# Kernel tuning notes

Measured on AMD Instinct MI355X. Metric: run time of the kernel, lower is better.

## Reference

```python
import jax, jax.numpy as jnp
import numpy as np

BS, P, D = 64, 300, 1024
NUM_CLASSES = 150


def setup_inputs() -> dict:
    key = jax.random.key(0)
    ks = jax.random.split(key, 12)
    s = 0.02
    return {
        "x": jax.random.normal(ks[0], (BS * P, D), jnp.float32),
        "subject": jax.random.normal(ks[1], (BS, D), jnp.float32),
        "obj": jax.random.normal(ks[2], (BS, D), jnp.float32),
        "relation": jax.random.normal(ks[3], (BS, D), jnp.float32),
        "W_theta": jax.random.normal(ks[4], (D, D), jnp.float32) * s,
        "b_theta": jax.random.normal(ks[5], (D,), jnp.float32) * s,
        "W_pair": jax.random.normal(ks[6], (3 * D, 1), jnp.float32) * s,
        "b_pair": jax.random.normal(ks[7], (1,), jnp.float32) * s,
        "W_cls": jax.random.normal(ks[8], (2 * D, 1), jnp.float32) * s,
        "b_cls": jax.random.normal(ks[9], (1,), jnp.float32) * s,
        "W_bbox": jax.random.normal(ks[10], (D, (NUM_CLASSES + 1) * 4), jnp.float32) * s,
        "b_bbox": jax.random.normal(ks[11], ((NUM_CLASSES + 1) * 4,), jnp.float32) * s,
    }


def reference(x, subject, obj, relation, W_theta, b_theta, W_pair, b_pair,
              W_cls, b_cls, W_bbox, b_bbox):
    bs = relation.shape[0]
    rel = relation @ W_theta + b_theta  # (bs, D)
    xb = x.reshape(bs, P, D)

    # cls_score_pair(concat([x1, x2, rel])) decomposed into 3 sliced matmuls.
    # x1[b,i,j] = x[b,j] (cols), x2[b,i,j] = x[b,i] (rows).
    Wa, Wb, Wc = W_pair[:D, 0], W_pair[D:2 * D, 0], W_pair[2 * D:, 0]
    col_term = xb @ Wa          # (bs, P) -> broadcast over rows i
    row_term = xb @ Wb          # (bs, P) -> broadcast over cols j
    rel_term = rel @ Wc + b_pair[0]  # (bs,)
    pair_score = jax.nn.sigmoid(row_term[:, :, None] + col_term[None if False else slice(None), None, :]
                                + rel_term[:, None, None])  # (bs, P, P)

    # cls_score on [x, subject] and [x, object]
    W1, W2 = W_cls[:D, 0], W_cls[D:, 0]
    xw = xb @ W1                                  # (bs, P)
    s_score = jax.nn.sigmoid(xw + (subject @ W2 + b_cls[0])[:, None])  # (bs, P)
    o_score = jax.nn.sigmoid(xw + (obj @ W2 + b_cls[0])[:, None])      # (bs, P)

    pair_score = pair_score * o_score[:, None, :] * s_score[:, :, None]

    x_subj = jnp.stack([1.0 - s_score, s_score], axis=-1).reshape(-1, 2)
    x_obj = jnp.stack([1.0 - o_score, o_score], axis=-1).reshape(-1, 2)

    bbox_deltas = x @ W_bbox + b_bbox  # (bs*P, (C+1)*4)
    return (x_subj, x_obj, pair_score, bbox_deltas)
```

## Files before the change

kernel.cpp:

```cpp
#include <hip/hip_runtime.h>

#define PP    300
#define DD    1024
#define NOUT  604
#define NROWS 19200
#define OFF_PAIR  76800
#define OFF_BBOX  5836800

typedef unsigned short u16;
typedef __attribute__((ext_vector_type(8))) short bf16x8;
typedef __attribute__((ext_vector_type(4))) float f32x4;

#define GLOBAL_AS __attribute__((address_space(1)))
#define LDS_AS    __attribute__((address_space(3)))

__device__ inline u16 f2bf(float f) {
    unsigned u = __float_as_uint(f);
    return (u16)((u + 0x7fffu + ((u >> 16) & 1u)) >> 16);
}
__device__ inline float dot4(float4 a, float4 b) {
    return fmaf(a.x, b.x, fmaf(a.y, b.y, fmaf(a.z, b.z, a.w * b.w)));
}
__device__ inline float sigmoidf(float z) { return 1.f / (1.f + __expf(-z)); }

__global__ void k_vtheta(const float* __restrict__ Wt, const float* __restrict__ Wpair,
                         float* __restrict__ v) {
    int wave = threadIdx.x >> 6, lane = threadIdx.x & 63;
    int k = blockIdx.x * 4 + wave;
    const float4* row = (const float4*)(Wt + (size_t)k * DD);
    const float4* wc  = (const float4*)(Wpair + 2 * DD);
    float s = 0.f;
#pragma unroll
    for (int i = 0; i < 4; ++i) s += dot4(row[i * 64 + lane], wc[i * 64 + lane]);
#pragma unroll
    for (int off = 32; off; off >>= 1) s += __shfl_down(s, off, 64);
    if (lane == 0) v[k] = s;
}

__global__ void k_scalars(const float* __restrict__ relation, const float* __restrict__ subject,
                          const float* __restrict__ obj, const float* __restrict__ btheta,
                          const float* __restrict__ Wpair, const float* __restrict__ bpair,
                          const float* __restrict__ Wcls, const float* __restrict__ bcls,
                          const float* __restrict__ v,
                          float* __restrict__ relt, float* __restrict__ subc,
                          float* __restrict__ objc) {
    __shared__ float red[4];
    int wave = threadIdx.x >> 6, lane = threadIdx.x & 63;
    int b = blockIdx.x;
    const float4* aa;
    const float4* bb;
    if (wave == 0)      { aa = (const float4*)(relation + (size_t)b * DD); bb = (const float4*)v; }
    else if (wave == 1) { aa = (const float4*)(subject + (size_t)b * DD);  bb = (const float4*)(Wcls + DD); }
    else if (wave == 2) { aa = (const float4*)(obj + (size_t)b * DD);      bb = (const float4*)(Wcls + DD); }
    else                { aa = (const float4*)btheta;                      bb = (const float4*)(Wpair + 2 * DD); }
    float s = 0.f;
#pragma unroll
    for (int i = 0; i < 4; ++i) s += dot4(aa[i * 64 + lane], bb[i * 64 + lane]);
#pragma unroll
    for (int off = 32; off; off >>= 1) s += __shfl_down(s, off, 64);
    if (lane == 0) red[wave] = s;
    __syncthreads();
    if (threadIdx.x == 0) {
        relt[b] = red[0] + red[3] + bpair[0];
        subc[b] = red[1] + bcls[0];
        objc[b] = red[2] + bcls[0];
    }
}

template<int WB>
__global__ __launch_bounds__(256) void k_rows_t(
        const float* __restrict__ x, const float* __restrict__ Wpair,
        const float* __restrict__ Wcls,
        const float* __restrict__ relt, const float* __restrict__ subc,
        const float* __restrict__ objc,
        float* __restrict__ colv, float* __restrict__ rowp,
        float* __restrict__ sarr, float* __restrict__ oarr,
        float* __restrict__ out, u16* __restrict__ xb,
        const float* __restrict__ Wbbox, u16* __restrict__ Bt) {
    __shared__ float tile[32][33];
    if (blockIdx.x >= 4800) {
        int blk = blockIdx.x - 4800;
        int tid = threadIdx.x;
        int k0 = (blk & 31) * 32;
        int n0 = (blk >> 5) * 32;
        int tx = tid & 31;
        int ty = tid >> 5;
#pragma unroll
        for (int i = 0; i < 4; ++i) {
            int k = k0 + ty + i * 8;
            int n = n0 + tx;
            tile[ty + i * 8][tx] = (n < NOUT) ? Wbbox[(size_t)k * NOUT + n] : 0.f;
        }
        __syncthreads();
#pragma unroll
        for (int i = 0; i < 4; ++i) {
            int n = n0 + ty + i * 8;
            int k = k0 + tx;
            Bt[(size_t)n * DD + k] = f2bf(tile[tx][ty + i * 8]);
        }
        return;
    }
    int wave = threadIdx.x >> 6, lane = threadIdx.x & 63;
    int r = blockIdx.x * 4 + wave;
    const float4* xr = (const float4*)(x + (size_t)r * DD);
    const float4* wa = (const float4*)(Wpair);
    const float4* wb = (const float4*)(Wpair + DD);
    const float4* w1 = (const float4*)(Wcls);
    float ca = 0.f, cb = 0.f, cw = 0.f;
#pragma unroll
    for (int i = 0; i < 4; ++i) {
        int idx = i * 64 + lane;
        float4 xv = xr[idx];
        ca += dot4(xv, wa[idx]);
        cb += dot4(xv, wb[idx]);
        cw += dot4(xv, w1[idx]);
        if (WB) {
            unsigned lo = __builtin_amdgcn_perm(__float_as_uint(xv.y), __float_as_uint(xv.x), 0x07060302u);
            unsigned hi = __builtin_amdgcn_perm(__float_as_uint(xv.w), __float_as_uint(xv.z), 0x07060302u);
            *(uint2*)(xb + (size_t)r * DD + idx * 4) = make_uint2(lo, hi);
        }
    }
#pragma unroll
    for (int off = 32; off; off >>= 1) {
        ca += __shfl_down(ca, off, 64);
        cb += __shfl_down(cb, off, 64);
        cw += __shfl_down(cw, off, 64);
    }
    if (lane == 0) {
        int b = r / 300;
        float s = sigmoidf(cw + subc[b]);
        float o = sigmoidf(cw + objc[b]);
        colv[r] = ca;
        rowp[r] = cb + relt[b];
        sarr[r] = s;
        oarr[r] = o;
        ((float2*)out)[r]         = make_float2(1.f - s, s);
        ((float2*)out)[NROWS + r] = make_float2(1.f - o, o);
    }
}

#define BKK 64
#define NSTEP 16

#define WAITCNT_VM(N) asm volatile("s_waitcnt vmcnt(" #N ")" ::: "memory")

#define STAGE_TILE(buf, k0)                                                                  \
    _Pragma("unroll")                                                                        \
    for (int q = 0; q < 4; ++q) {                                                            \
        int rowblk = q * 32 + wave * 8;                                                      \
        const u16* ga = a_base + (size_t)(rowblk + s_row) * DD + (k0) + s_c16 * 8;           \
        __builtin_amdgcn_global_load_lds((const GLOBAL_AS unsigned int*)ga,                  \
                                         (LDS_AS unsigned int*)(As[buf] + rowblk * BKK),     \
                                         16, 0, 0);                                          \
        const u16* gb = b_base + (size_t)(rowblk + s_row) * DD + (k0) + s_c16 * 8;           \
        __builtin_amdgcn_global_load_lds((const GLOBAL_AS unsigned int*)gb,                  \
                                         (LDS_AS unsigned int*)(Bs[buf] + rowblk * BKK),     \
                                         16, 0, 0);                                          \
    }

#define COMPUTE_TILE(buf)                                                                    \
    _Pragma("unroll")                                                                        \
    for (int kk = 0; kk < BKK; kk += 32) {                                                   \
        bf16x8 af[4], bfv[4];                                                                \
        int cx = (((kk >> 3) + quad) ^ (l16 & 7)) * 8;                                       \
        _Pragma("unroll")                                                                    \
        for (int f = 0; f < 4; ++f) {                                                        \
            int m = wr * 64 + f * 16 + l16;                                                  \
            af[f] = *(const bf16x8*)(As[buf] + m * BKK + cx);                                \
            int n = wc * 64 + f * 16 + l16;                                                  \
            bfv[f] = *(const bf16x8*)(Bs[buf] + n * BKK + cx);                               \
        }                                                                                    \
        _Pragma("unroll")                                                                    \
        for (int fi = 0; fi < 4; ++fi)                                                       \
            _Pragma("unroll")                                                                \
            for (int fj = 0; fj < 4; ++fj)                                                   \
                acc[fi][fj] = __builtin_amdgcn_mfma_f32_16x16x32_bf16(                       \
                    af[fi], bfv[fj], acc[fi][fj], 0, 0, 0);                                  \
    }

__global__ __launch_bounds__(256) void k_fused(
        const u16* __restrict__ xb, const u16* __restrict__ bt,
        const float* __restrict__ bias, float* __restrict__ outb,
        const float* __restrict__ rowp, const float* __restrict__ colv,
        const float* __restrict__ sarr, const float* __restrict__ oarr,
        float* __restrict__ pout) {
    __shared__ u16 As[2][128 * BKK] __attribute__((aligned(16)));
    __shared__ u16 Bs[2][128 * BKK] __attribute__((aligned(16)));

    int gbid = blockIdx.x;
    if (gbid < 760) {
        int xcd = gbid & 7;
        int rest = gbid >> 3;
        int n_t = rest % 5;
        int m_t = (rest / 5) * 8 + xcd;
        if (m_t >= 150) return;

        int tid = threadIdx.x;
        int wave = tid >> 6;
        int lane = tid & 63;
        int wr = wave >> 1, wc = wave & 1;
        int quad = lane >> 4;
        int l16 = lane & 15;

        f32x4 acc[4][4] = {};

        const u16* a_base = xb + (size_t)m_t * 128 * DD;
        const u16* b_base = bt + (size_t)n_t * 128 * DD;
        int s_row = lane >> 3;
        int s_c16 = (lane & 7) ^ s_row;

        STAGE_TILE(0, 0)

#pragma unroll 1
        for (int t = 0; t < NSTEP; t += 2) {
            STAGE_TILE(1, (t + 1) * BKK)
            WAITCNT_VM(8);
            __builtin_amdgcn_s_barrier();
            COMPUTE_TILE(0)
            __builtin_amdgcn_s_barrier();
            if (t + 2 < NSTEP) {
                STAGE_TILE(0, (t + 2) * BKK)
                WAITCNT_VM(8);
            } else {
                WAITCNT_VM(0);
            }
            __builtin_amdgcn_s_barrier();
            COMPUTE_TILE(1)
            __builtin_amdgcn_s_barrier();
        }

#pragma unroll
        for (int fj = 0; fj < 4; ++fj) {
            int col = n_t * 128 + wc * 64 + fj * 16 + l16;
            if (col < NOUT) {
                float bia = bias[col];
#pragma unroll
                for (int fi = 0; fi < 4; ++fi) {
#pragma unroll
                    for (int rg = 0; rg < 4; ++rg) {
                        int row = m_t * 128 + wr * 64 + fi * 16 + quad * 4 + rg;
                        outb[(size_t)row * NOUT + col] = acc[fi][fj][rg] + bia;
                    }
                }
            }
        }
    } else {
        float* cb_s = (float*)As;
        float* ob_s = ((float*)As) + 300;
        int blk = gbid - 760;
        int b = blk / 30;
        int chunk = blk - b * 30;
        int r0 = b * 300 + chunk * 10;
        int tid = threadIdx.x;
        for (int j = tid; j < 300; j += 256) {
            cb_s[j] = colv[b * 300 + j];
            ob_s[j] = oarr[b * 300 + j];
        }
        __syncthreads();
        if (tid < 150) {
            float c0 = cb_s[2 * tid], c1 = cb_s[2 * tid + 1];
            float o0 = ob_s[2 * tid], o1 = ob_s[2 * tid + 1];
#pragma unroll
            for (int rr = 0; rr < 10; ++rr) {
                int r = r0 + rr;
                float rp = rowp[r];
                float ss = sarr[r];
                float p0 = sigmoidf(rp + c0) * o0 * ss;
                float p1 = sigmoidf(rp + c1) * o1 * ss;
                ((float2*)(pout + (size_t)r * 300))[tid] = make_float2(p0, p1);
            }
        }
    }
}

__global__ __launch_bounds__(256) void k_prep(const float* __restrict__ Wbbox, u16* __restrict__ Bt,
                                              const float* __restrict__ Wt, const float* __restrict__ Wpair,
                                              float* __restrict__ v) {
    __shared__ float tile[32][33];
    int blk = blockIdx.x;
    int tid = threadIdx.x;
    if (blk < 640) {
        int k0 = (blk & 31) * 32;
        int n0 = (blk >> 5) * 32;
        int tx = tid & 31;
        int ty = tid >> 5;
#pragma unroll
        for (int i = 0; i < 4; ++i) {
            int k = k0 + ty + i * 8;
            int n = n0 + tx;
            tile[ty + i * 8][tx] = (n < NOUT) ? Wbbox[(size_t)k * NOUT + n] : 0.f;
        }
        __syncthreads();
#pragma unroll
        for (int i = 0; i < 4; ++i) {
            int n = n0 + ty + i * 8;
            int k = k0 + tx;
            Bt[(size_t)n * DD + k] = f2bf(tile[tx][ty + i * 8]);
        }
    } else {
        int wave = tid >> 6, lane = tid & 63;
        int k = (blk - 640) * 4 + wave;
        const float4* row = (const float4*)(Wt + (size_t)k * DD);
        const float4* wc  = (const float4*)(Wpair + 2 * DD);
        float s = 0.f;
#pragma unroll
        for (int i = 0; i < 4; ++i) s += dot4(row[i * 64 + lane], wc[i * 64 + lane]);
#pragma unroll
        for (int off = 32; off; off >>= 1) s += __shfl_down(s, off, 64);
        if (lane == 0) v[k] = s;
    }
}

__global__ __launch_bounds__(192) void k_pair_sa(
        const float* __restrict__ rowp, const float* __restrict__ colv,
        const float* __restrict__ sarr, const float* __restrict__ oarr,
        float* __restrict__ pout) {
    __shared__ float cb_s[300];
    __shared__ float ob_s[300];
    int blk = blockIdx.x;
    int b = blk / 30;
    int chunk = blk - b * 30;
    int r0 = b * 300 + chunk * 10;
    int tid = threadIdx.x;
    for (int j = tid; j < 300; j += 192) {
        cb_s[j] = colv[b * 300 + j];
        ob_s[j] = oarr[b * 300 + j];
    }
    __syncthreads();
    if (tid < 150) {
        float c0 = cb_s[2 * tid], c1 = cb_s[2 * tid + 1];
        float o0 = ob_s[2 * tid], o1 = ob_s[2 * tid + 1];
#pragma unroll
        for (int rr = 0; rr < 10; ++rr) {
            int r = r0 + rr;
            float rp = rowp[r];
            float ss = sarr[r];
            float p0 = sigmoidf(rp + c0) * o0 * ss;
            float p1 = sigmoidf(rp + c1) * o1 * ss;
            ((float2*)(pout + (size_t)r * 300))[tid] = make_float2(p0, p1);
        }
    }
}

__global__ __launch_bounds__(256) void k_gemm(
        const float* __restrict__ x, const u16* __restrict__ bt,
        const float* __restrict__ bias, float* __restrict__ out) {
    __shared__ u16 As[128 * BKK] __attribute__((aligned(16)));
    __shared__ u16 Bs[128 * BKK] __attribute__((aligned(16)));

    int bid = blockIdx.x;
    int xcd = bid & 7;
    int rest = bid >> 3;
    int n_t = rest % 5;
    int m_t = (rest / 5) * 8 + xcd;
    if (m_t >= 150) return;

    int tid = threadIdx.x;
    int wave = tid >> 6;
    int lane = tid & 63;
    int wr = wave >> 1, wc = wave & 1;
    int quad = lane >> 4;
    int l16 = lane & 15;

    f32x4 acc[4][4] = {};

    const float* a_base = x  + (size_t)m_t * 128 * DD;
    const u16*   b_base = bt + (size_t)n_t * 128 * DD;
    int s_row = lane >> 3;
    int s_c16 = lane & 7;
    int arow8 = tid >> 4;
    int acol4 = tid & 15;

    for (int k0 = 0; k0 < DD; k0 += BKK) {
#pragma unroll
        for (int q = 0; q < 4; ++q) {
            int rowblk = q * 32 + wave * 8;
            const u16* gb = b_base + (size_t)(rowblk + s_row) * DD + k0 + s_c16 * 8;
            __builtin_amdgcn_global_load_lds((const GLOBAL_AS unsigned int*)gb,
                                             (LDS_AS unsigned int*)(Bs + rowblk * BKK),
                                             16, 0, 0);
        }
#pragma unroll
        for (int it = 0; it < 8; ++it) {
            int row = it * 16 + arow8;
            float4 av = *(const float4*)(a_base + (size_t)row * DD + k0 + acol4 * 4);
            unsigned lo = __builtin_amdgcn_perm(__float_as_uint(av.y), __float_as_uint(av.x), 0x07060302u);
            unsigned hi = __builtin_amdgcn_perm(__float_as_uint(av.w), __float_as_uint(av.z), 0x07060302u);
            *(uint2*)(As + row * BKK + acol4 * 4) = make_uint2(lo, hi);
        }
        __syncthreads();
#pragma unroll
        for (int kk = 0; kk < BKK; kk += 32) {
            bf16x8 af[4], bfv[4];
#pragma unroll
            for (int f = 0; f < 4; ++f) {
                int m = wr * 64 + f * 16 + l16;
                af[f] = *(const bf16x8*)(As + m * BKK + kk + quad * 8);
                int n = wc * 64 + f * 16 + l16;
                bfv[f] = *(const bf16x8*)(Bs + n * BKK + kk + quad * 8);
            }
#pragma unroll
            for (int fi = 0; fi < 4; ++fi)
#pragma unroll
                for (int fj = 0; fj < 4; ++fj)
                    acc[fi][fj] = __builtin_amdgcn_mfma_f32_16x16x32_bf16(
                        af[fi], bfv[fj], acc[fi][fj], 0, 0, 0);
        }
        __syncthreads();
    }

#pragma unroll
    for (int fj = 0; fj < 4; ++fj) {
        int col = n_t * 128 + wc * 64 + fj * 16 + l16;
        if (col < NOUT) {
            float bia = bias[col];
#pragma unroll
            for (int fi = 0; fi < 4; ++fi) {
#pragma unroll
                for (int rg = 0; rg < 4; ++rg) {
                    int row = m_t * 128 + wr * 64 + fi * 16 + quad * 4 + rg;
                    out[(size_t)row * NOUT + col] = acc[fi][fj][rg] + bia;
                }
            }
        }
    }
}

extern "C" void kernel_launch(void* const* d_in, const int* in_sizes, int n_in,
                              void* d_out, int out_size, void* d_ws, size_t ws_size,
                              hipStream_t stream) {
    const void* P[12] = {};
    int sv[3] = {-1, -1, -1}; int nsv = 0;
    int sc[2] = {-1, -1};     int nsc = 0;
    for (int i = 0; i < n_in; ++i) {
        switch (in_sizes[i]) {
            case 19660800: P[0]  = d_in[i]; break;
            case 65536:    if (nsv < 3) sv[nsv++] = i; break;
            case 1048576:  P[4]  = d_in[i]; break;
            case 1024:     P[5]  = d_in[i]; break;
            case 3072:     P[6]  = d_in[i]; break;
            case 1:        if (nsc < 2) sc[nsc++] = i; break;
            case 2048:     P[8]  = d_in[i]; break;
            case 618496:   P[10] = d_in[i]; break;
            case 604:      P[11] = d_in[i]; break;
            default: break;
        }
    }
    bool alpha = (n_in == 12 && in_sizes[0] == 618496);
    if (alpha) {
        P[2] = d_in[sv[0]]; P[3] = d_in[sv[1]]; P[1] = d_in[sv[2]];
        P[9] = d_in[sc[0]]; P[7] = d_in[sc[1]];
    } else {
        P[1] = d_in[sv[0]]; P[2] = d_in[sv[1]]; P[3] = d_in[sv[2]];
        P[7] = d_in[sc[0]]; P[9] = d_in[sc[1]];
    }
    const float* x        = (const float*)P[0];
    const float* subject  = (const float*)P[1];
    const float* obj      = (const float*)P[2];
    const float* relation = (const float*)P[3];
    const float* W_theta  = (const float*)P[4];
    const float* b_theta  = (const float*)P[5];
    const float* W_pair   = (const float*)P[6];
    const float* b_pair   = (const float*)P[7];
    const float* W_cls    = (const float*)P[8];
    const float* b_cls    = (const float*)P[9];
    const float* W_bbox   = (const float*)P[10];
    const float* b_bbox   = (const float*)P[11];
    float* out = (float*)d_out;

    char* ws = (char*)d_ws;
    float* v    = (float*)(ws + 0);
    float* relt = (float*)(ws + 4096);
    float* subc = (float*)(ws + 4352);
    float* objc = (float*)(ws + 4608);
    float* colv = (float*)(ws + 4864);
    float* rowp = (float*)(ws + 81664);
    float* sarr = (float*)(ws + 158464);
    float* oarr = (float*)(ws + 235264);
    u16*   Bt   = (u16*)(ws + 312064);
    u16*   Xb   = (u16*)(ws + 1622784);

    const size_t WS_NEED_BF16 = 40944384;
    bool big_ws = (ws_size >= WS_NEED_BF16);

    if (big_ws) {
        k_vtheta<<<256, 256, 0, stream>>>(W_theta, W_pair, v);
        k_scalars<<<64, 256, 0, stream>>>(relation, subject, obj, b_theta, W_pair, b_pair,
                                          W_cls, b_cls, v, relt, subc, objc);
        k_rows_t<1><<<5440, 256, 0, stream>>>(x, W_pair, W_cls, relt, subc, objc,
                                              colv, rowp, sarr, oarr, out, Xb, W_bbox, Bt);
        k_fused<<<2680, 256, 0, stream>>>(Xb, Bt, b_bbox, out + OFF_BBOX,
                                          rowp, colv, sarr, oarr, out + OFF_PAIR);
    } else {
        k_prep<<<896, 256, 0, stream>>>(W_bbox, Bt, W_theta, W_pair, v);
        k_scalars<<<64, 256, 0, stream>>>(relation, subject, obj, b_theta, W_pair, b_pair,
                                          W_cls, b_cls, v, relt, subc, objc);
        k_rows_t<0><<<4800, 256, 0, stream>>>(x, W_pair, W_cls, relt, subc, objc,
                                              colv, rowp, sarr, oarr, out, nullptr, W_bbox, Bt);
        k_pair_sa<<<1920, 192, 0, stream>>>(rowp, colv, sarr, oarr, out + OFF_PAIR);
        k_gemm<<<760, 256, 0, stream>>>(x, Bt, b_bbox, out + OFF_BBOX);
    }
}
```

Baseline: 204.7 us.

## Merge vtheta into row pass and defer sigmoid scoring to fused kernel

The row-reduction kernel no longer depends on the per-batch scalars. It now stores the raw cw dot product, and the W_theta·Wc reduction is folded into it as extra blocks, which removes one kernel launch from the big-workspace path. The sigmoid subject/object scores and the x_subj/x_obj outputs are now computed inside the pair branch of the fused GEMM kernel from cw, relt, subc and objc. This shortens the dependency chain but recomputes sigmoids per block and adds work to the fused kernel.

Result: no change. 202.9 us, median of 2 (-0.9%).

```diff
diff --git a/kernel.cpp b/kernel.cpp
--- a/kernel.cpp
+++ b/kernel.cpp
@@ -23,18 +23,78 @@
 }
 __device__ inline float sigmoidf(float z) { return 1.f / (1.f + __expf(-z)); }
 
-__global__ void k_vtheta(const float* __restrict__ Wt, const float* __restrict__ Wpair,
-                         float* __restrict__ v) {
+__global__ __launch_bounds__(256) void k_rows_raw(
+        const float* __restrict__ x, const float* __restrict__ Wpair,
+        const float* __restrict__ Wcls,
+        float* __restrict__ colv, float* __restrict__ rowp,
+        float* __restrict__ cwv, u16* __restrict__ xb,
+        const float* __restrict__ Wbbox, u16* __restrict__ Bt,
+        const float* __restrict__ Wt, float* __restrict__ v) {
+    __shared__ float tile[32][33];
+    if (blockIdx.x >= 5440) {
+        int wave = threadIdx.x >> 6, lane = threadIdx.x & 63;
+        int k = (blockIdx.x - 5440) * 4 + wave;
+        const float4* row = (const float4*)(Wt + (size_t)k * DD);
+        const float4* wc  = (const float4*)(Wpair + 2 * DD);
+        float s = 0.f;
+#pragma unroll
+        for (int i = 0; i < 4; ++i) s += dot4(row[i * 64 + lane], wc[i * 64 + lane]);
+#pragma unroll
+        for (int off = 32; off; off >>= 1) s += __shfl_down(s, off, 64);
+        if (lane == 0) v[k] = s;
+        return;
+    }
+    if (blockIdx.x >= 4800) {
+        int blk = blockIdx.x - 4800;
+        int tid = threadIdx.x;
+        int k0 = (blk & 31) * 32;
+        int n0 = (blk >> 5) * 32;
+        int tx = tid & 31;
+        int ty = tid >> 5;
+#pragma unroll
+        for (int i = 0; i < 4; ++i) {
+            int k = k0 + ty + i * 8;
+            int n = n0 + tx;
+            tile[ty + i * 8][tx] = (n < NOUT) ? Wbbox[(size_t)k * NOUT + n] : 0.f;
+        }
+        __syncthreads();
+#pragma unroll
+        for (int i = 0; i < 4; ++i) {
+            int n = n0 + ty + i * 8;
+            int k = k0 + tx;
+            Bt[(size_t)n * DD + k] = f2bf(tile[tx][ty + i * 8]);
+        }
+        return;
+    }
     int wave = threadIdx.x >> 6, lane = threadIdx.x & 63;
-    int k = blockIdx.x * 4 + wave;
-    const float4* row = (const float4*)(Wt + (size_t)k * DD);
-    const float4* wc  = (const float4*)(Wpair + 2 * DD);
-    float s = 0.f;
-#pragma unroll
-    for (int i = 0; i < 4; ++i) s += dot4(row[i * 64 + lane], wc[i * 64 + lane]);
-#pragma unroll
-    for (int off = 32; off; off >>= 1) s += __shfl_down(s, off, 64);
-    if (lane == 0) v[k] = s;
+    int r = blockIdx.x * 4 + wave;
+    const float4* xr = (const float4*)(x + (size_t)r * DD);
+    const float4* wa = (const float4*)(Wpair);
+    const float4* wb = (const float4*)(Wpair + DD);
+    const float4* w1 = (const float4*)(Wcls);
+    float ca = 0.f, cb = 0.f, cw = 0.f;
+#pragma unroll
+    for (int i = 0; i < 4; ++i) {
+        int idx = i * 64 + lane;
+        float4 xv = xr[idx];
+        ca += dot4(xv, wa[idx]);
+        cb += dot4(xv, wb[idx]);
+        cw += dot4(xv, w1[idx]);
+        unsigned lo = __builtin_amdgcn_perm(__float_as_uint(xv.y), __float_as_uint(xv.x), 0x07060302u);
+        unsigned hi = __builtin_amdgcn_perm(__float_as_uint(xv.w), __float_as_uint(xv.z), 0x07060302u);
+        *(uint2*)(xb + (size_t)r * DD + idx * 4) = make_uint2(lo, hi);
+    }
+#pragma unroll
+    for (int off = 32; off; off >>= 1) {
+        ca += __shfl_down(ca, off, 64);
+        cb += __shfl_down(cb, off, 64);
+        cw += __shfl_down(cw, off, 64);
+    }
+    if (lane == 0) {
+        colv[r] = ca;
+        rowp[r] = cb;
+        cwv[r]  = cw;
+    }
 }
 
 __global__ void k_scalars(const float* __restrict__ relation, const float* __restrict__ subject,
@@ -64,78 +124,6 @@
         relt[b] = red[0] + red[3] + bpair[0];
         subc[b] = red[1] + bcls[0];
         objc[b] = red[2] + bcls[0];
-    }
-}
-
-template<int WB>
-__global__ __launch_bounds__(256) void k_rows_t(
-        const float* __restrict__ x, const float* __restrict__ Wpair,
-        const float* __restrict__ Wcls,
-        const float* __restrict__ relt, const float* __restrict__ subc,
-        const float* __restrict__ objc,
-        float* __restrict__ colv, float* __restrict__ rowp,
-        float* __restrict__ sarr, float* __restrict__ oarr,
-        float* __restrict__ out, u16* __restrict__ xb,
-        const float* __restrict__ Wbbox, u16* __restrict__ Bt) {
-    __shared__ float tile[32][33];
-    if (blockIdx.x >= 4800) {
-        int blk = blockIdx.x - 4800;
-        int tid = threadIdx.x;
-        int k0 = (blk & 31) * 32;
-        int n0 = (blk >> 5) * 32;
-        int tx = tid & 31;
-        int ty = tid >> 5;
-#pragma unroll
-        for (int i = 0; i < 4; ++i) {
-            int k = k0 + ty + i * 8;
-            int n = n0 + tx;
-            tile[ty + i * 8][tx] = (n < NOUT) ? Wbbox[(size_t)k * NOUT + n] : 0.f;
-        }
-        __syncthreads();
-#pragma unroll
-        for (int i = 0; i < 4; ++i) {
-            int n = n0 + ty + i * 8;
-            int k = k0 + tx;
-            Bt[(size_t)n * DD + k] = f2bf(tile[tx][ty + i * 8]);
-        }
-        return;
-    }
-    int wave = threadIdx.x >> 6, lane = threadIdx.x & 63;
-    int r = blockIdx.x * 4 + wave;
-    const float4* xr = (const float4*)(x + (size_t)r * DD);
-    const float4* wa = (const float4*)(Wpair);
-    const float4* wb = (const float4*)(Wpair + DD);
-    const float4* w1 = (const float4*)(Wcls);
-    float ca = 0.f, cb = 0.f, cw = 0.f;
-#pragma unroll
-    for (int i = 0; i < 4; ++i) {
-        int idx = i * 64 + lane;
-        float4 xv = xr[idx];
-        ca += dot4(xv, wa[idx]);
-        cb += dot4(xv, wb[idx]);
-        cw += dot4(xv, w1[idx]);
-        if (WB) {
-            unsigned lo = __builtin_amdgcn_perm(__float_as_uint(xv.y), __float_as_uint(xv.x), 0x07060302u);
-            unsigned hi = __builtin_amdgcn_perm(__float_as_uint(xv.w), __float_as_uint(xv.z), 0x07060302u);
-            *(uint2*)(xb + (size_t)r * DD + idx * 4) = make_uint2(lo, hi);
-        }
-    }
-#pragma unroll
-    for (int off = 32; off; off >>= 1) {
-        ca += __shfl_down(ca, off, 64);
-        cb += __shfl_down(cb, off, 64);
-        cw += __shfl_down(cw, off, 64);
-    }
-    if (lane == 0) {
-        int b = r / 300;
-        float s = sigmoidf(cw + subc[b]);
-        float o = sigmoidf(cw + objc[b]);
-        colv[r] = ca;
-        rowp[r] = cb + relt[b];
-        sarr[r] = s;
-        oarr[r] = o;
-        ((float2*)out)[r]         = make_float2(1.f - s, s);
-        ((float2*)out)[NROWS + r] = make_float2(1.f - o, o);
     }
 }
 
@@ -182,8 +170,10 @@
         const u16* __restrict__ xb, const u16* __restrict__ bt,
         const float* __restrict__ bias, float* __restrict__ outb,
         const float* __restrict__ rowp, const float* __restrict__ colv,
-        const float* __restrict__ sarr, const float* __restrict__ oarr,
-        float* __restrict__ pout) {
+        const float* __restrict__ cwv,
+        const float* __restrict__ relt, const float* __restrict__ subc,
+        const float* __restrict__ objc,
+        float* __restrict__ outx, float* __restrict__ pout) {
     __shared__ u16 As[2][128 * BKK] __attribute__((aligned(16)));
     __shared__ u16 Bs[2][128 * BKK] __attribute__((aligned(16)));
 
@@ -247,14 +237,18 @@
     } else {
         float* cb_s = (float*)As;
         float* ob_s = ((float*)As) + 300;
+        float* cw_s = ((float*)As) + 600;
         int blk = gbid - 760;
         int b = blk / 30;
         int chunk = blk - b * 30;
         int r0 = b * 300 + chunk * 10;
         int tid = threadIdx.x;
+        float relt_b = relt[b], subc_b = subc[b], objc_b = objc[b];
         for (int j = tid; j < 300; j += 256) {
             cb_s[j] = colv[b * 300 + j];
-            ob_s[j] = oarr[b * 300 + j];
+            float cwj = cwv[b * 300 + j];
+            cw_s[j] = cwj;
+            ob_s[j] = sigmoidf(cwj + objc_b);
         }
         __syncthreads();
         if (tid < 150) {
@@ -263,12 +257,21 @@
 #pragma unroll
             for (int rr = 0; rr < 10; ++rr) {
                 int r = r0 + rr;
-                float rp = rowp[r];
-                float ss = sarr[r];
+                int lr = chunk * 10 + rr;
+                float rp = rowp[r] + relt_b;
+                float ss = sigmoidf(cw_s[lr] + subc_b);
                 float p0 = sigmoidf(rp + c0) * o0 * ss;
                 float p1 = sigmoidf(rp + c1) * o1 * ss;
                 ((float2*)(pout + (size_t)r * 300))[tid] = make_float2(p0, p1);
             }
+        } else if (tid < 160) {
+            int rr = tid - 150;
+            int r = r0 + rr;
+            int lr = chunk * 10 + rr;
+            float sv = sigmoidf(cw_s[lr] + subc_b);
+            float ov = sigmoidf(cw_s[lr] + objc_b);
+            ((float2*)outx)[r]         = make_float2(1.f - sv, sv);
+            ((float2*)outx)[NROWS + r] = make_float2(1.f - ov, ov);
         }
     }
 }
@@ -308,6 +311,48 @@
 #pragma unroll
         for (int off = 32; off; off >>= 1) s += __shfl_down(s, off, 64);
         if (lane == 0) v[k] = s;
+    }
+}
+
+__global__ __launch_bounds__(256) void k_rows_sa(
+        const float* __restrict__ x, const float* __restrict__ Wpair,
+        const float* __restrict__ Wcls,
+        const float* __restrict__ relt, const float* __restrict__ subc,
+        const float* __restrict__ objc,
+        float* __restrict__ colv, float* __restrict__ rowp,
+        float* __restrict__ sarr, float* __restrict__ oarr,
+        float* __restrict__ out) {
+    int wave = threadIdx.x >> 6, lane = threadIdx.x & 63;
+    int r = blockIdx.x * 4 + wave;
+    const float4* xr = (const float4*)(x + (size_t)r * DD);
+    const float4* wa = (const float4*)(Wpair);
+    const float4* wb = (const float4*)(Wpair + DD);
+    const float4* w1 = (const float4*)(Wcls);
+    float ca = 0.f, cb = 0.f, cw = 0.f;
+#pragma unroll
+    for (int i = 0; i < 4; ++i) {
+        int idx = i * 64 + lane;
+        float4 xv = xr[idx];
+        ca += dot4(xv, wa[idx]);
+        cb += dot4(xv, wb[idx]);
+        cw += dot4(xv, w1[idx]);
+    }
+#pragma unroll
+    for (int off = 32; off; off >>= 1) {
+        ca += __shfl_down(ca, off, 64);
+        cb += __shfl_down(cb, off, 64);
+        cw += __shfl_down(cw, off, 64);
+    }
+    if (lane == 0) {
+        int b = r / 300;
+        float s = sigmoidf(cw + subc[b]);
+        float o = sigmoidf(cw + objc[b]);
+        colv[r] = ca;
+        rowp[r] = cb + relt[b];
+        sarr[r] = s;
+        oarr[r] = o;
+        ((float2*)out)[r]         = make_float2(1.f - s, s);
+        ((float2*)out)[NROWS + r] = make_float2(1.f - o, o);
     }
 }
 
@@ -475,7 +520,7 @@
     float* objc = (float*)(ws + 4608);
     float* colv = (float*)(ws + 4864);
     float* rowp = (float*)(ws + 81664);
-    float* sarr = (float*)(ws + 158464);
+    float* cwv  = (float*)(ws + 158464);
     float* oarr = (float*)(ws + 235264);
     u16*   Bt   = (u16*)(ws + 312064);
     u16*   Xb   = (u16*)(ws + 1622784);
@@ -484,20 +529,20 @@
     bool big_ws = (ws_size >= WS_NEED_BF16);
 
     if (big_ws) {
-        k_vtheta<<<256, 256, 0, stream>>>(W_theta, W_pair, v);
+        k_rows_raw<<<5696, 256, 0, stream>>>(x, W_pair, W_cls, colv, rowp, cwv, Xb,
+                                             W_bbox, Bt, W_theta, v);
         k_scalars<<<64, 256, 0, stream>>>(relation, subject, obj, b_theta, W_pair, b_pair,
                                           W_cls, b_cls, v, relt, subc, objc);
-        k_rows_t<1><<<5440, 256, 0, stream>>>(x, W_pair, W_cls, relt, subc, objc,
-                                              colv, rowp, sarr, oarr, out, Xb, W_bbox, Bt);
         k_fused<<<2680, 256, 0, stream>>>(Xb, Bt, b_bbox, out + OFF_BBOX,
-                                          rowp, colv, sarr, oarr, out + OFF_PAIR);
+                                          rowp, colv, cwv, relt, subc, objc,
+                                          out, out + OFF_PAIR);
     } else {
         k_prep<<<896, 256, 0, stream>>>(W_bbox, Bt, W_theta, W_pair, v);
         k_scalars<<<64, 256, 0, stream>>>(relation, subject, obj, b_theta, W_pair, b_pair,
                                           W_cls, b_cls, v, relt, subc, objc);
-        k_rows_t<0><<<4800, 256, 0, stream>>>(x, W_pair, W_cls, relt, subc, objc,
-                                              colv, rowp, sarr, oarr, out, nullptr, W_bbox, Bt);
-        k_pair_sa<<<1920, 192, 0, stream>>>(rowp, colv, sarr, oarr, out + OFF_PAIR);
+        k_rows_sa<<<4800, 256, 0, stream>>>(x, W_pair, W_cls, relt, subc, objc,
+                                            colv, rowp, cwv, oarr, out);
+        k_pair_sa<<<1920, 192, 0, stream>>>(rowp, colv, cwv, oarr, out + OFF_PAIR);
         k_gemm<<<760, 256, 0, stream>>>(x, Bt, b_bbox, out + OFF_BBOX);
     }
 }
```
